# Performance work log

Measured on AMD Instinct MI355X. Metric: run time of the kernel, lower is better.

Reference implementation:

```python
import jax, jax.numpy as jnp
import numpy as np
from jax import lax

DIM = 128
HEADS = 2
SR = 4
HID = 512  # 4 * DIM
DROPKEY_P = 0.1


def _ln(x, g, b, eps=1e-5):
    m = jnp.mean(x, axis=-1, keepdims=True)
    v = jnp.var(x, axis=-1, keepdims=True)
    return (x - m) / jnp.sqrt(v + eps) * g + b


def _block(x, H, W, params, key):
    (n1g, n1b, qw, kvw, srw, srb, sng, snb, pw, pb,
     n2g, n2b, f1w, f1b, dww, dwb, f2w, f2b) = params
    B, N, C = x.shape
    dh = C // HEADS
    scale = dh ** -0.5
    # --- spatial-reduction attention ---
    h = _ln(x, n1g, n1b)
    q = (h @ qw.T).reshape(B, N, HEADS, dh).transpose(0, 2, 1, 3)  # [B,h,N,dh]
    xi = h.transpose(0, 2, 1).reshape(B, C, H, W)
    xs = lax.conv_general_dilated(xi, srw, (SR, SR), 'VALID',
                                  dimension_numbers=('NCHW', 'OIHW', 'NCHW'))
    xs = xs + srb[None, :, None, None]
    Np = (H // SR) * (W // SR)
    xs = xs.reshape(B, C, Np).transpose(0, 2, 1)  # [B,N',C]
    xs = _ln(xs, sng, snb)
    kv = (xs @ kvw.T).reshape(B, Np, 2, HEADS, dh).transpose(2, 0, 3, 1, 4)
    k, v = kv[0], kv[1]  # [B,h,N',dh]
    attn = jnp.einsum('bhnd,bhmd->bhnm', q, k) * scale
    # dropkey: bernoulli(p) mask pushed to -1e12 before softmax (always applied)
    mask = jax.random.bernoulli(key, DROPKEY_P, attn.shape)
    attn = attn + mask.astype(attn.dtype) * (-1e12)
    attn = jax.nn.softmax(attn, axis=-1)
    o = jnp.einsum('bhnm,bhmd->bhnd', attn, v).transpose(0, 2, 1, 3).reshape(B, N, C)
    x = x + o @ pw.T + pb
    # --- MLP with depthwise conv ---
    h2 = _ln(x, n2g, n2b)
    h2 = h2 @ f1w.T + f1b  # [B,N,HID]
    hi = h2.transpose(0, 2, 1).reshape(B, HID, H, W)
    hi = lax.conv_general_dilated(hi, dww, (1, 1), 'SAME',
                                  feature_group_count=HID,
                                  dimension_numbers=('NCHW', 'OIHW', 'NCHW'))
    hi = hi + dwb[None, :, None, None]
    h2 = hi.reshape(B, HID, N).transpose(0, 2, 1)
    h2 = jax.nn.gelu(h2, approximate=False)
    x = x + h2 @ f2w.T + f2b
    return x


def setup_inputs() -> dict:
    key = jax.random.key(0)
    ks = jax.random.split(key, 10)
    p = {}
    p['x'] = jax.random.normal(ks[0], (16, 2 * DIM, 56, 56), jnp.float32)
    p['concat_w'] = jax.random.normal(ks[1], (DIM, 2 * DIM), jnp.float32) * 0.02
    p['concat_b'] = jnp.zeros((DIM,), jnp.float32)
    # two Blocks -> leading dim 2 on all per-block params
    p['norm1_g'] = jnp.ones((2, DIM), jnp.float32)
    p['norm1_b'] = jnp.zeros((2, DIM), jnp.float32)
    p['q_w'] = jax.random.normal(ks[2], (2, DIM, DIM), jnp.float32) * 0.02
    p['kv_w'] = jax.random.normal(ks[3], (2, 2 * DIM, DIM), jnp.float32) * 0.02
    p['sr_w'] = jax.random.normal(ks[4], (2, DIM, DIM, SR, SR), jnp.float32) * 0.03
    p['sr_b'] = jnp.zeros((2, DIM), jnp.float32)
    p['srn_g'] = jnp.ones((2, DIM), jnp.float32)
    p['srn_b'] = jnp.zeros((2, DIM), jnp.float32)
    p['proj_w'] = jax.random.normal(ks[5], (2, DIM, DIM), jnp.float32) * 0.02
    p['proj_b'] = jnp.zeros((2, DIM), jnp.float32)
    p['norm2_g'] = jnp.ones((2, DIM), jnp.float32)
    p['norm2_b'] = jnp.zeros((2, DIM), jnp.float32)
    p['fc1_w'] = jax.random.normal(ks[6], (2, HID, DIM), jnp.float32) * 0.02
    p['fc1_b'] = jnp.zeros((2, HID), jnp.float32)
    p['dw_w'] = jax.random.normal(ks[7], (2, HID, 1, 3, 3), jnp.float32) * 0.1
    p['dw_b'] = jnp.zeros((2, HID), jnp.float32)
    p['fc2_w'] = jax.random.normal(ks[8], (2, DIM, HID), jnp.float32) * 0.02
    p['fc2_b'] = jnp.zeros((2, DIM), jnp.float32)
    return p


def reference(x, concat_w, concat_b, norm1_g, norm1_b, q_w, kv_w, sr_w, sr_b,
              srn_g, srn_b, proj_w, proj_b, norm2_g, norm2_b, fc1_w, fc1_b,
              dw_w, dw_b, fc2_w, fc2_b):
    b, c, h, w = x.shape
    xs = x.transpose(0, 2, 3, 1).reshape(b, h * w, c)
    xs = xs @ concat_w.T + concat_b  # [B,N,DIM]
    mkey = jax.random.key(42)
    stacked = (norm1_g, norm1_b, q_w, kv_w, sr_w, sr_b, srn_g, srn_b, proj_w,
               proj_b, norm2_g, norm2_b, fc1_w, fc1_b, dw_w, dw_b, fc2_w, fc2_b)
    for i in range(2):
        params_i = tuple(p[i] for p in stacked)
        xs = _block(xs, h, w, params_i, jax.random.fold_in(mkey, i))
    return xs.reshape(b, h, w, DIM).transpose(0, 3, 1, 2)
```

## Files before the change

kernel.cpp:

```cpp
#include <hip/hip_runtime.h>
#include <stdint.h>

typedef __attribute__((ext_vector_type(8))) short short8;
typedef __attribute__((ext_vector_type(4))) float f32x4;
typedef __attribute__((ext_vector_type(2))) float f32x2;
typedef unsigned short u16;
typedef uint32_t u32;
typedef unsigned long long u64;

__host__ __device__ static inline void threefry(u32 k0, u32 k1, u32 x0, u32 x1,
                                                u32* o0, u32* o1) {
  u32 ks2 = k0 ^ k1 ^ 0x1BD11BDAu;
  x0 += k0; x1 += k1;
#define TF_RR(r) { x0 += x1; x1 = (x1 << (r)) | (x1 >> (32 - (r))); x1 ^= x0; }
  TF_RR(13) TF_RR(15) TF_RR(26) TF_RR(6)
  x0 += k1;  x1 += ks2 + 1u;
  TF_RR(17) TF_RR(29) TF_RR(16) TF_RR(24)
  x0 += ks2; x1 += k0 + 2u;
  TF_RR(13) TF_RR(15) TF_RR(26) TF_RR(6)
  x0 += k0;  x1 += k1 + 3u;
  TF_RR(17) TF_RR(29) TF_RR(16) TF_RR(24)
  x0 += k1;  x1 += ks2 + 4u;
  TF_RR(13) TF_RR(15) TF_RR(26) TF_RR(6)
  x0 += ks2; x1 += k0 + 5u;
#undef TF_RR
  *o0 = x0; *o1 = x1;
}

__device__ static inline float bf2f(u16 u) {
  union { u32 i; float f; } v; v.i = ((u32)u) << 16; return v.f;
}
__device__ static inline u16 f2bf(float f) {
  union { float f; u32 i; } v; v.f = f;
  u32 x = v.i;
  return (u16)((x + 0x7FFFu + ((x >> 16) & 1u)) >> 16);
}
__device__ static inline float lo_bf(u32 w) {
  union { u32 i; float f; } v; v.i = w << 16; return v.f;
}
__device__ static inline float hi_bf(u32 w) {
  union { u32 i; float f; } v; v.i = w & 0xFFFF0000u; return v.f;
}
__device__ static inline bool is_f32(const u32* ng) { return ng[0] == 0x3F800000u; }

typedef const uint32_t __attribute__((address_space(1)))* gas_ptr;
typedef uint32_t __attribute__((address_space(3)))* las_ptr;
__device__ static inline void gld16(const u16* g, u16* l) {
  __builtin_amdgcn_global_load_lds((gas_ptr)(const void*)g, (las_ptr)(void*)l, 16, 0, 0);
}

#define MASK_HALF 9834496u

__global__ __launch_bounds__(256) void mask_gen2(u32* __restrict__ MSK2, u32 k0, u32 k1) {
  int t = blockIdx.x * 256 + threadIdx.x;
  if (t >= 351232) return;
  int w = t % 7;
  int rowbh = t / 7;
  u32 base = (u32)rowbh * 196u + (u32)w * 32u;
  int kmax = 196 - w * 32;
  if (kmax > 32) kmax = 32;
  u32 bits0 = 0, bits1 = 0;
  for (int j = 0; j < kmax; j++) {
    u32 o0, o1;
    threefry(k0, k1, base + (u32)j, base + (u32)j + MASK_HALF, &o0, &o1);
    union { u32 u; float f; } u0, u1;
    u0.u = (o0 >> 9) | 0x3F800000u;
    u1.u = (o1 >> 9) | 0x3F800000u;
    if (u0.f - 1.0f < 0.1f) bits0 |= (1u << j);
    if (u1.f - 1.0f < 0.1f) bits1 |= (1u << j);
  }
  MSK2[(size_t)rowbh * 7 + w] = bits0;
  MSK2[(size_t)(rowbh + 50176) * 7 + w] = bits1;
}

struct PtrTab { const void* p[20]; };
#define ARENA_N 963968
#define VT_WORDS 229376

__global__ __launch_bounds__(256) void convert_params(PtrTab tab, u16* __restrict__ arena,
                                                      u32* __restrict__ VT) {
  const int cum[21] = {0, 32768, 32896, 33152, 33408, 66176, 131712, 656000, 656256,
                       656512, 656768, 689536, 689792, 690048, 690304, 821376, 822400,
                       831616, 832640, 963712, 963968};
  int idx = blockIdx.x * 256 + threadIdx.x;
  if (idx >= ARENA_N) {
    int v = idx - ARENA_N;
    if (v < VT_WORDS) VT[v] = 0;
    return;
  }
  bool f32m = (((const u32*)tab.p[2])[0] == 0x3F800000u);
  int t = 0;
  while (idx >= cum[t + 1]) t++;
  int local = idx - cum[t];
  if (t == 16) {
    int blk = local / 4608, r = local - blk * 4608;
    int wi = r >> 9, c = r & 511;
    local = blk * 4608 + c * 9 + wi;
  }
  u16 v;
  if (f32m) v = f2bf(((const float*)tab.p[t])[local]);
  else      v = ((const u16*)tab.p[t])[local];
  arena[idx] = v;
}

__global__ __launch_bounds__(256) void transpose_in(const void* __restrict__ Xin,
                                                    const u32* __restrict__ ng,
                                                    u16* __restrict__ Xt) {
  bool f32m = is_f32(ng);
  __shared__ u16 tile[64][65];
  int n0 = blockIdx.x * 64, c0 = blockIdx.y * 64, b = blockIdx.z;
  int tx = threadIdx.x & 63, ty = threadIdx.x >> 6;
  if (f32m) {
    const float* src = (const float*)Xin + (size_t)b * 256 * 3136;
#pragma unroll
    for (int i = 0; i < 16; i++) {
      int cl = i * 4 + ty;
      tile[cl][tx] = f2bf(src[(size_t)(c0 + cl) * 3136 + n0 + tx]);
    }
  } else {
    const u16* src = (const u16*)Xin + (size_t)b * 256 * 3136;
#pragma unroll
    for (int i = 0; i < 16; i++) {
      int cl = i * 4 + ty;
      tile[cl][tx] = src[(size_t)(c0 + cl) * 3136 + n0 + tx];
    }
  }
  __syncthreads();
  u16* dst = Xt + (size_t)b * 3136 * 256;
#pragma unroll
  for (int i = 0; i < 16; i++) {
    int nl = i * 4 + ty;
    dst[(size_t)(n0 + nl) * 256 + c0 + tx] = tile[tx][nl];
  }
}

__global__ __launch_bounds__(256) void transpose_out(const float* __restrict__ X,
                                                     const u32* __restrict__ ng,
                                                     void* __restrict__ Out) {
  bool f32m = is_f32(ng);
  __shared__ float tile[64][65];
  int n0 = blockIdx.x * 64, d0 = blockIdx.y * 64, b = blockIdx.z;
  int tx = threadIdx.x & 63, ty = threadIdx.x >> 6;
#pragma unroll
  for (int i = 0; i < 16; i++) {
    int nl = i * 4 + ty;
    tile[nl][tx] = X[((size_t)b * 3136 + n0 + nl) * 128 + d0 + tx];
  }
  __syncthreads();
#pragma unroll
  for (int i = 0; i < 16; i++) {
    int dl = i * 4 + ty;
    size_t o = ((size_t)b * 128 + d0 + dl) * 3136 + n0 + tx;
    if (f32m) ((float*)Out)[o] = tile[tx][dl];
    else      ((u16*)Out)[o]   = f2bf(tile[tx][dl]);
  }
}

__global__ __launch_bounds__(256) void im2col_sr(const u16* __restrict__ H,
                                                 u16* __restrict__ Acol) {
  int t = blockIdx.x * 256 + threadIdx.x;
  int c = t & 127;
  int rest = t >> 7;
  int ij = rest & 15;
  int row = rest >> 4;
  int i = ij >> 2, j = ij & 3;
  int bb = row / 196, pp = row - bb * 196;
  int ph = pp / 14, pw = pp - ph * 14;
  int n = (4 * ph + i) * 56 + 4 * pw + j;
  Acol[(size_t)row * 2048 + c * 16 + ij] = H[((size_t)bb * 3136 + n) * 128 + c];
}

__global__ __launch_bounds__(256) __attribute__((amdgpu_waves_per_eu(2, 4)))
void gemm_tiled(const u16* __restrict__ A,
                const u16* __restrict__ W,
                const u16* __restrict__ bias,
                float* __restrict__ outF,
                u16* __restrict__ outB,
                u16* __restrict__ outVT,
                int M, int N, int K, int mode) {
  __shared__ __align__(16) u16 smem[16896];
  u16* AlsP = smem;
  u16* BlsP = smem + 8192;
  int n0 = blockIdx.y * 128, m0 = blockIdx.x * 128;
  int tid = threadIdx.x, wv = tid >> 6, lane = tid & 63;
  int wr = wv >> 1, wc = wv & 1;
  int l15 = lane & 15, hh = lane >> 4, lk = hh * 8;
  int srow = wv * 32 + (lane >> 2);
  int scol = (lane & 3) * 8;

  f32x4 acc[4][4];
#pragma unroll
  for (int m = 0; m < 4; m++)
#pragma unroll
    for (int n = 0; n < 4; n++) acc[m][n] = (f32x4){0.f, 0.f, 0.f, 0.f};

#define STAGE(buf, k0)                                                          \
  {                                                                             \
    _Pragma("unroll") for (int i = 0; i < 2; i++) {                             \
      int ar = m0 + srow + i * 16;                                              \
      if (ar >= M) ar = M - 1;                                                  \
      gld16(A + (size_t)ar * K + (k0) + scol,                                   \
            AlsP + (buf) * 4096 + (wv * 32 + i * 16) * 32);                     \
      int br = n0 + srow + i * 16;                                              \
      gld16(W + (size_t)br * K + (k0) + scol,                                   \
            BlsP + (buf) * 4096 + (wv * 32 + i * 16) * 32);                     \
    }                                                                           \
  }

  int nt = K >> 5;
  STAGE(0, 0);
  int cur = 0;
  for (int t = 0; t < nt; t++) {
    __syncthreads();
    if (t + 1 < nt) STAGE(cur ^ 1, (t + 1) * 32);
    short8 af[4], bf[4];
#pragma unroll
    for (int m = 0; m < 4; m++)
      af[m] = *(const short8*)(AlsP + cur * 4096 + (wr * 64 + m * 16 + l15) * 32 + lk);
#pragma unroll
    for (int n = 0; n < 4; n++)
      bf[n] = *(const short8*)(BlsP + cur * 4096 + (wc * 64 + n * 16 + l15) * 32 + lk);
#pragma unroll
    for (int m = 0; m < 4; m++)
#pragma unroll
      for (int n = 0; n < 4; n++)
        acc[m][n] = __builtin_amdgcn_mfma_f32_16x16x32_bf16(af[m], bf[n], acc[m][n], 0, 0, 0);
    cur ^= 1;
  }
#undef STAGE

  if (mode == 0) {
    __syncthreads();
#pragma unroll
    for (int n = 0; n < 4; n++) {
      int col = wc * 64 + n * 16 + l15;
      float bv = bias ? bf2f(bias[n0 + col]) : 0.0f;
#pragma unroll
      for (int m = 0; m < 4; m++) {
        int rbase = wr * 64 + m * 16 + hh * 4;
#pragma unroll
        for (int r = 0; r < 4; r++)
          smem[(rbase + r) * 132 + col] = f2bf(acc[m][n][r] + bv);
      }
    }
    __syncthreads();
#pragma unroll
    for (int p = 0; p < 8; p++) {
      int row = p * 16 + (tid >> 4);
      int colb = (tid & 15) * 8;
      int grow = m0 + row;
      if (grow < M) {
        short8 v = *(const short8*)&smem[row * 132 + colb];
        *(short8*)(outB + (size_t)grow * N + n0 + colb) = v;
      }
    }
    return;
  }

#pragma unroll
  for (int n = 0; n < 4; n++) {
    int col = n0 + wc * 64 + n * 16 + l15;
    float bv = bias ? bf2f(bias[col]) : 0.0f;
#pragma unroll
    for (int m = 0; m < 4; m++) {
      int rbase = m0 + wr * 64 + m * 16 + hh * 4;
#pragma unroll
      for (int r = 0; r < 4; r++) {
        int row = rbase + r;
        if (row < M) {
          float v = acc[m][n][r] + bv;
          if (mode == 1) outF[(size_t)row * N + col] = v;
          else if (mode == 2) outF[(size_t)row * N + col] += v;
          else {
            if (col < 128) outB[(size_t)row * 128 + col] = f2bf(v);
            else {
              int hd = (col - 128) >> 6, d = (col - 128) & 63;
              int b = row / 196, key = row - b * 196;
              outVT[(size_t)((b * 2 + hd) * 64 + d) * 224 + key] = f2bf(v);
            }
          }
        }
      }
    }
  }
}

__global__ __launch_bounds__(256) __attribute__((amdgpu_waves_per_eu(2, 4)))
void gemm_n128(const u16* __restrict__ A,
               const u16* __restrict__ W,
               const u16* __restrict__ bias,
               float* __restrict__ outF,
               u16* __restrict__ outB,
               const u16* __restrict__ lnG,
               const u16* __restrict__ lnB,
               u16* __restrict__ outH,
               int M, int K, int mode) {
  __shared__ __align__(16) u16 smem[12288];
  __shared__ float sumsA[64][4];
  __shared__ float sumsB[64][4];
  u16* Als = smem;
  u16* Bls = smem + 4096;
  int m0 = blockIdx.y * 64;
  int tid = threadIdx.x, wv = tid >> 6, lane = tid & 63;
  int l15 = lane & 15, hq = lane >> 4, lk = hq * 8;
  int scol = (lane & 3) * 8;

  f32x4 acc[4][2];
#pragma unroll
  for (int m = 0; m < 4; m++)
#pragma unroll
    for (int n = 0; n < 2; n++) acc[m][n] = (f32x4){0.f, 0.f, 0.f, 0.f};

#define STAGE(buf, k0)                                                          \
  {                                                                             \
    int ar = m0 + wv * 16 + (lane >> 2);                                        \
    if (ar >= M) ar = M - 1;                                                    \
    gld16(A + (size_t)ar * K + (k0) + scol, Als + (buf) * 2048 + wv * 512);     \
    _Pragma("unroll") for (int i = 0; i < 2; i++) {                             \
      int br = wv * 32 + i * 16 + (lane >> 2);                                  \
      gld16(W + (size_t)br * K + (k0) + scol,                                   \
            Bls + (buf) * 4096 + wv * 1024 + i * 512);                          \
    }                                                                           \
  }

  int nt = K >> 5;
  STAGE(0, 0);
  int cur = 0;
  for (int t = 0; t < nt; t++) {
    __syncthreads();
    if (t + 1 < nt) STAGE(cur ^ 1, (t + 1) * 32);
    short8 af[4], bf[2];
#pragma unroll
    for (int m = 0; m < 4; m++)
      af[m] = *(const short8*)(Als + cur * 2048 + (m * 16 + l15) * 32 + lk);
#pragma unroll
    for (int n = 0; n < 2; n++)
      bf[n] = *(const short8*)(Bls + cur * 4096 + (wv * 32 + n * 16 + l15) * 32 + lk);
#pragma unroll
    for (int m = 0; m < 4; m++)
#pragma unroll
      for (int n = 0; n < 2; n++)
        acc[m][n] = __builtin_amdgcn_mfma_f32_16x16x32_bf16(af[m], bf[n], acc[m][n], 0, 0, 0);
    cur ^= 1;
  }
#undef STAGE

  if (mode == 2) {
#pragma unroll
    for (int n = 0; n < 2; n++) {
      int col = wv * 32 + n * 16 + l15;
      float bv = bias ? bf2f(bias[col]) : 0.0f;
#pragma unroll
      for (int m = 0; m < 4; m++) {
        int rbase = m0 + m * 16 + hq * 4;
#pragma unroll
        for (int r = 0; r < 4; r++)
          outF[(size_t)(rbase + r) * 128 + col] += acc[m][n][r] + bv;
      }
    }
    return;
  }

  if (mode >= 4) {
#pragma unroll
    for (int n = 0; n < 2; n++) {
      int col = wv * 32 + n * 16 + l15;
      float bv = bias ? bf2f(bias[col]) : 0.0f;
#pragma unroll
      for (int m = 0; m < 4; m++) {
        int rbase = m0 + m * 16 + hq * 4;
#pragma unroll
        for (int r = 0; r < 4; r++) {
          float v = acc[m][n][r] + bv;
          if (mode == 5) v += outF[(size_t)(rbase + r) * 128 + col];
          acc[m][n][r] = v;
          outF[(size_t)(rbase + r) * 128 + col] = v;
        }
      }
    }
#pragma unroll
    for (int m = 0; m < 4; m++) {
#pragma unroll
      for (int r = 0; r < 4; r++) {
        float a = acc[m][0][r] + acc[m][1][r];
        float b = acc[m][0][r] * acc[m][0][r] + acc[m][1][r] * acc[m][1][r];
#pragma unroll
        for (int d = 1; d < 16; d <<= 1) {
          a += __shfl_xor(a, d);
          b += __shfl_xor(b, d);
        }
        if (l15 == 0) {
          int lrow = m * 16 + hq * 4 + r;
          sumsA[lrow][wv] = a;
          sumsB[lrow][wv] = b;
        }
      }
    }
    __syncthreads();
#pragma unroll
    for (int m = 0; m < 4; m++) {
#pragma unroll
      for (int r = 0; r < 4; r++) {
        int lrow = m * 16 + hq * 4 + r;
        float t1 = sumsA[lrow][0] + sumsA[lrow][1] + sumsA[lrow][2] + sumsA[lrow][3];
        float t2 = sumsB[lrow][0] + sumsB[lrow][1] + sumsB[lrow][2] + sumsB[lrow][3];
        float mean = t1 * 0.0078125f;
        float var = t2 * 0.0078125f - mean * mean;
        float inv = 1.0f / sqrtf(var + 1e-5f);
#pragma unroll
        for (int n = 0; n < 2; n++) {
          int col = wv * 32 + n * 16 + l15;
          float g = bf2f(lnG[col]), bb2 = bf2f(lnB[col]);
          smem[lrow * 132 + col] = f2bf((acc[m][n][r] - mean) * inv * g + bb2);
        }
      }
    }
    __syncthreads();
#pragma unroll
    for (int p = 0; p < 4; p++) {
      int row = p * 16 + (tid >> 4);
      int colb = (tid & 15) * 8;
      short8 v = *(const short8*)&smem[row * 132 + colb];
      *(short8*)(outH + (size_t)(m0 + row) * 128 + colb) = v;
    }
    return;
  }

  __syncthreads();
#pragma unroll
  for (int n = 0; n < 2; n++) {
    int col = wv * 32 + n * 16 + l15;
    float bv = bias ? bf2f(bias[col]) : 0.0f;
#pragma unroll
    for (int m = 0; m < 4; m++) {
      int rbase = m * 16 + hq * 4;
#pragma unroll
      for (int r = 0; r < 4; r++)
        smem[(rbase + r) * 132 + col] = f2bf(acc[m][n][r] + bv);
    }
  }
  __syncthreads();
#pragma unroll
  for (int p = 0; p < 4; p++) {
    int row = p * 16 + (tid >> 4);
    int colb = (tid & 15) * 8;
    short8 v = *(const short8*)&smem[row * 132 + colb];
    *(short8*)(outB + (size_t)(m0 + row) * 128 + colb) = v;
  }
}

__global__ __launch_bounds__(256) void gemm_splitk(const u16* __restrict__ A,
                                                   const u16* __restrict__ W,
                                                   float* __restrict__ PS,
                                                   int M, int N, int K) {
  __shared__ __align__(16) u16 Als[2][4096];
  __shared__ __align__(16) u16 Bls[2][4096];
  int n0 = blockIdx.x * 128, m0 = blockIdx.y * 128, ks = blockIdx.z;
  int tid = threadIdx.x, wv = tid >> 6, lane = tid & 63;
  int wr = wv >> 1, wc = wv & 1;
  int l15 = lane & 15, lk = (lane >> 4) * 8;
  int srow = wv * 32 + (lane >> 2);
  int scol = (lane & 3) * 8;

  f32x4 acc[4][4];
#pragma unroll
  for (int m = 0; m < 4; m++)
#pragma unroll
    for (int n = 0; n < 4; n++) acc[m][n] = (f32x4){0.f, 0.f, 0.f, 0.f};

#define STAGE(buf, k0)                                                          \
  {                                                                             \
    _Pragma("unroll") for (int i = 0; i < 2; i++) {                             \
      int ar = m0 + srow + i * 16;                                              \
      if (ar >= M) ar = M - 1;                                                  \
      gld16(A + (size_t)ar * K + (k0) + scol,                                   \
            &Als[buf][(wv * 32 + i * 16) * 32]);                                \
      int br = n0 + srow + i * 16;                                              \
      gld16(W + (size_t)br * K + (k0) + scol,                                   \
            &Bls[buf][(wv * 32 + i * 16) * 32]);                                \
    }                                                                           \
  }

  int kbeg = ks * 128;
  STAGE(0, kbeg);
  int cur = 0;
  for (int t = 0; t < 4; t++) {
    __syncthreads();
    if (t + 1 < 4) STAGE(cur ^ 1, kbeg + (t + 1) * 32);
    short8 af[4], bf[4];
#pragma unroll
    for (int m = 0; m < 4; m++)
      af[m] = *(const short8*)(&Als[cur][(wr * 64 + m * 16 + l15) * 32 + lk]);
#pragma unroll
    for (int n = 0; n < 4; n++)
      bf[n] = *(const short8*)(&Bls[cur][(wc * 64 + n * 16 + l15) * 32 + lk]);
#pragma unroll
    for (int m = 0; m < 4; m++)
#pragma unroll
      for (int n = 0; n < 4; n++)
        acc[m][n] = __builtin_amdgcn_mfma_f32_16x16x32_bf16(af[m], bf[n], acc[m][n], 0, 0, 0);
    cur ^= 1;
  }
#undef STAGE

  float* myPS = PS + (size_t)ks * M * N;
#pragma unroll
  for (int n = 0; n < 4; n++) {
    int col = n0 + wc * 64 + n * 16 + l15;
#pragma unroll
    for (int m = 0; m < 4; m++) {
      int rbase = m0 + wr * 64 + m * 16 + (lane >> 4) * 4;
#pragma unroll
      for (int r = 0; r < 4; r++) {
        int row = rbase + r;
        if (row < M) myPS[(size_t)row * N + col] = acc[m][n][r];
      }
    }
  }
}

__global__ __launch_bounds__(256) void splitk_reduce_ln(const float* __restrict__ PS,
                                                        const u16* __restrict__ bias,
                                                        const u16* __restrict__ G,
                                                        const u16* __restrict__ Bi,
                                                        u16* __restrict__ XSN) {
  __shared__ float red[4][2];
  int tid = threadIdx.x;
  int row = blockIdx.x * 2 + (tid >> 7);
  int col = tid & 127;
  int t = row * 128 + col;
  float s = bf2f(bias[col]);
#pragma unroll
  for (int k = 0; k < 16; k++) s += PS[(size_t)k * 401408 + t];
  float s1 = s, s2 = s * s;
#pragma unroll
  for (int d = 1; d < 64; d <<= 1) {
    s1 += __shfl_xor(s1, d);
    s2 += __shfl_xor(s2, d);
  }
  int wv = tid >> 6;
  if ((tid & 63) == 0) { red[wv][0] = s1; red[wv][1] = s2; }
  __syncthreads();
  int other = wv ^ 1;
  float t1 = red[wv][0] + red[other][0];
  float t2 = red[wv][1] + red[other][1];
  float mean = t1 * 0.0078125f;
  float var = t2 * 0.0078125f - mean * mean;
  float inv = 1.0f / sqrtf(var + 1e-5f);
  XSN[t] = f2bf((s - mean) * inv * bf2f(G[col]) + bf2f(Bi[col]));
}

__global__ __launch_bounds__(256) __attribute__((amdgpu_waves_per_eu(2, 4)))
void attn_kernel(const u16* __restrict__ Q,
                 const u16* __restrict__ Kb,
                 const u16* __restrict__ VT,
                 const u32* __restrict__ M2,
                 u16* __restrict__ O) {
  __shared__ __align__(16) u16 smA[14848];
  int t = blockIdx.x;
  int tp = (t & 7) * 196 + (t >> 3);
  int bh = tp / 49, qt = tp - bh * 49;
  int b = bh >> 1, hd = bh & 1;
  int q0 = qt * 64;
  int tid = threadIdx.x;

  int wv = tid >> 6, lane = tid & 63;
  int l15 = lane & 15, h = lane >> 4, lk = h * 8;

  {
    const u16* ksrc = Kb + (size_t)b * 196 * 128 + hd * 64;
    for (int idx = tid; idx < 1568; idx += 256) {
      int row = idx >> 3, ch = idx & 7;
      short8 v = *(const short8*)(ksrc + (size_t)row * 128 + ch * 8);
      *(short8*)&smA[row * 68 + ch * 8] = v;
    }
  }

  const u16* qp = Q + ((size_t)(b * 3136 + q0 + wv * 16 + l15) * 128) + hd * 64 + lk;
  short8 aq0 = *(const short8*)(qp);
  short8 aq1 = *(const short8*)(qp + 32);
  int rowg = q0 + wv * 16 + h * 4;

  u32 mwv[4][7];
  const u32* mwbase = M2 + (size_t)(bh * 3136 + rowg) * 7;
#pragma unroll
  for (int r = 0; r < 4; r++)
#pragma unroll
    for (int w = 0; w < 7; w++) mwv[r][w] = mwbase[r * 7 + w];

  __syncthreads();

  float sarr[13][4];
#pragma unroll
  for (int cc = 0; cc < 13; cc++) {
    int key = cc * 16 + l15;
    int keyc = key > 195 ? 195 : key;
    short8 kb0 = *(const short8*)&smA[keyc * 68 + lk];
    short8 kb1 = *(const short8*)&smA[keyc * 68 + 32 + lk];
    f32x4 s = {0.f, 0.f, 0.f, 0.f};
    s = __builtin_amdgcn_mfma_f32_16x16x32_bf16(aq0, kb0, s, 0, 0, 0);
    s = __builtin_amdgcn_mfma_f32_16x16x32_bf16(aq1, kb1, s, 0, 0, 0);
#pragma unroll
    for (int r = 0; r < 4; r++) sarr[cc][r] = s[r] * 0.125f;
  }

#pragma unroll
  for (int cc = 0; cc < 13; cc++) {
    bool keyok = (cc * 16 + l15) < 196;
    int pos = (cc & 3) * 16 + l15;
#pragma unroll
    for (int r = 0; r < 4; r++) {
      u64 mm = (cc < 4) ? ((u64)mwv[r][0] | ((u64)mwv[r][1] << 32))
             : (cc < 8) ? ((u64)mwv[r][2] | ((u64)mwv[r][3] << 32))
             : (cc < 12) ? ((u64)mwv[r][4] | ((u64)mwv[r][5] << 32))
                         : ((u64)mwv[r][6]);
      bool drop = (mm >> pos) & 1ull;
      if (!keyok || drop) sarr[cc][r] = -3.0e38f;
    }
  }

  float mx[4] = {sarr[0][0], sarr[0][1], sarr[0][2], sarr[0][3]};
#pragma unroll
  for (int cc = 1; cc < 13; cc++)
#pragma unroll
    for (int r = 0; r < 4; r++) mx[r] = fmaxf(mx[r], sarr[cc][r]);
#pragma unroll
  for (int d = 1; d < 16; d <<= 1)
#pragma unroll
    for (int r = 0; r < 4; r++) mx[r] = fmaxf(mx[r], __shfl_xor(mx[r], d));
  float sm[4] = {0.f, 0.f, 0.f, 0.f};
#pragma unroll
  for (int cc = 0; cc < 13; cc++)
#pragma unroll
    for (int r = 0; r < 4; r++) {
      float p = __expf(sarr[cc][r] - mx[r]);
      sarr[cc][r] = p;
      sm[r] += p;
    }
#pragma unroll
  for (int d = 1; d < 16; d <<= 1)
#pragma unroll
    for (int r = 0; r < 4; r++) sm[r] += __shfl_xor(sm[r], d);
  float inv[4];
#pragma unroll
  for (int r = 0; r < 4; r++)
    asm("v_rcp_f32 %0, %1" : "=v"(inv[r]) : "v"(sm[r]));

  __syncthreads();

#pragma unroll
  for (int cc = 0; cc < 13; cc++)
#pragma unroll
    for (int r = 0; r < 4; r++)
      smA[(wv * 16 + h * 4 + r) * 232 + cc * 16 + l15] = f2bf(sarr[cc][r] * inv[r]);
#pragma unroll
  for (int rj = 0; rj < 4; rj++) smA[(wv * 16 + l15) * 232 + 208 + h * 4 + rj] = 0;

  const u16* vbase = VT + (size_t)(bh * 64) * 224;
  short8 vw[4];
#pragma unroll
  for (int i = 0; i < 4; i++) {
    vw[i] = *(const short8*)(vbase + (size_t)(0 * 16 + l15) * 224 + i * 32 + lk);
  }
#pragma unroll
  for (int dc = 0; dc < 4; dc++) {
    f32x4 oa = {0.f, 0.f, 0.f, 0.f};
#pragma unroll
    for (int kc = 0; kc < 7; kc++) {
      int i = dc * 7 + kc;
      short8 bv = vw[i & 3];
      if (i + 4 < 28) {
        int i2 = i + 4;
        int dc2 = i2 / 7, kc2 = i2 - dc2 * 7;
        vw[i & 3] =
            *(const short8*)(vbase + (size_t)(dc2 * 16 + l15) * 224 + kc2 * 32 + lk);
      }
      short8 a = *(const short8*)&smA[(wv * 16 + l15) * 232 + kc * 32 + lk];
      oa = __builtin_amdgcn_mfma_f32_16x16x32_bf16(a, bv, oa, 0, 0, 0);
    }
#pragma unroll
    for (int r = 0; r < 4; r++) {
      O[((size_t)(b * 3136 + rowg + r) * 128) + hd * 64 + dc * 16 + l15] = f2bf(oa[r]);
    }
  }
}

__global__ __launch_bounds__(256) __attribute__((amdgpu_waves_per_eu(2, 4)))
void dwconv_gelu(const u16* __restrict__ H2,
                 const u16* __restrict__ Wdw,
                 const u16* __restrict__ Bdw,
                 u16* __restrict__ Out) {
  int tid = threadIdx.x;
  int wv = tid >> 6, lane = tid & 63;
  int sb = blockIdx.x;
  int wg = (sb & 7) * 392 + (sb >> 3);
  int strip = wg * 4 + wv;
  int bb = strip / 784;
  int s = strip - bb * 784;
  int y = s / 14, x0 = (s - y * 14) * 4;
  int c0 = lane * 8;

  f32x2 wf[9][4];
#pragma unroll
  for (int t9 = 0; t9 < 9; t9++) {
    short8 w8 = *(const short8*)(Wdw + t9 * 512 + c0);
#pragma unroll
    for (int p = 0; p < 4; p++) {
      u32 w = ((const u32*)&w8)[p];
      wf[t9][p] = (f32x2){lo_bf(w), hi_bf(w)};
    }
  }
  f32x2 acc[4][4];
  {
    short8 b8 = *(const short8*)(Bdw + c0);
#pragma unroll
    for (int p = 0; p < 4; p++) {
      u32 w = ((const u32*)&b8)[p];
      f32x2 bv = {lo_bf(w), hi_bf(w)};
#pragma unroll
      for (int q = 0; q < 4; q++) acc[q][p] = bv;
    }
  }

  const u16* base = H2 + ((size_t)bb * 3136) * 512 + c0;
#pragma unroll
  for (int di = -1; di <= 1; di++) {
    int y2 = y + di;
    if (y2 < 0 || y2 >= 56) continue;
    const u16* rowp = base + (size_t)(y2 * 56) * 512;
#pragma unroll
    for (int j = 0; j < 6; j++) {
      int c = x0 - 1 + j;
      if (c < 0 || c > 55) continue;
      short8 h8 = *(const short8*)(rowp + (size_t)c * 512);
      f32x2 hf[4];
#pragma unroll
      for (int p = 0; p < 4; p++) {
        u32 w = ((const u32*)&h8)[p];
        hf[p] = (f32x2){lo_bf(w), hi_bf(w)};
      }
      int wrow = (di + 1) * 3;
#pragma unroll
      for (int q = 0; q < 4; q++) {
        int dx = j - 1 - q;
        if (dx < -1 || dx > 1) continue;
#pragma unroll
        for (int p = 0; p < 4; p++) acc[q][p] += hf[p] * wf[wrow + dx + 1][p];
      }
    }
  }

  size_t obase = ((size_t)(bb * 3136 + y * 56 + x0)) * 512 + c0;
#pragma unroll
  for (int q = 0; q < 4; q++) {
    short8 ov;
#pragma unroll
    for (int p = 0; p < 4; p++) {
      float g2[2];
#pragma unroll
      for (int e = 0; e < 2; e++) {
        float v = acc[q][p][e];
        float tt = v * v;
        float yn = v * (-2.3022088f - 0.1029434f * tt);
        float ex;
        asm("v_exp_f32 %0, %1" : "=v"(ex) : "v"(yn));
        float den = 1.0f + ex;
        float sg;
        asm("v_rcp_f32 %0, %1" : "=v"(sg) : "v"(den));
        g2[e] = v * sg;
      }
      u32 pk;
      asm("v_cvt_pk_bf16_f32 %0, %1, %2" : "=v"(pk) : "v"(g2[0]), "v"(g2[1]));
      ((u32*)&ov)[p] = pk;
    }
    *(short8*)(Out + obase + (size_t)q * 512) = ov;
  }
}

__global__ __launch_bounds__(256) void fill_sentinel(void* __restrict__ Out,
                                                     const u32* __restrict__ ng, int n) {
  bool f32m = is_f32(ng);
  int t = blockIdx.x * 256 + threadIdx.x;
  if (t >= n) return;
  if (f32m) ((float*)Out)[t] = 12345.0f;
  else      ((u16*)Out)[t]   = f2bf(12345.0f);
}

extern "C" void kernel_launch(void* const* d_in, const int* in_sizes, int n_in,
                              void* d_out, int out_size, void* d_ws, size_t ws_size,
                              hipStream_t stream) {
  (void)in_sizes; (void)n_in;
  const u32* ng = (const u32*)d_in[3];

  const size_t o_X   = 0;
  const size_t o_H   = 25690112;
  const size_t o_R   = o_H + 12845056;
  const size_t o_Q   = o_R;
  const size_t o_O   = o_R + 12845056;
  const size_t o_Xt  = o_R + 25690112;
  const size_t o_H2C = o_R;
  const size_t o_H2  = o_R + 51380224;
  const size_t o_XSN = o_H2 + 51380224;
  const size_t o_KB  = o_XSN + 802816;
  const size_t o_VT  = o_KB + 802816;
  const size_t o_M2  = o_VT + 917504;
  const size_t o_AR  = o_M2 + 2809856;
  const size_t NEED  = o_AR + (size_t)ARENA_N * 2;

  if (ws_size < NEED) {
    fill_sentinel<<<(out_size + 255) / 256, 256, 0, stream>>>(d_out, ng, out_size);
    return;
  }

  char* ws = (char*)d_ws;
  float* X  = (float*)(ws + o_X);
  u16* H    = (u16*)(ws + o_H);
  u16* Qb   = (u16*)(ws + o_Q);
  u16* Ob   = (u16*)(ws + o_O);
  u16* Xt   = (u16*)(ws + o_Xt);
  u16* H2C  = (u16*)(ws + o_H2C);
  u16* H2   = (u16*)(ws + o_H2);
  float* PS = (float*)(ws + o_H2);
  u16* XSN  = (u16*)(ws + o_XSN);
  u16* Kb   = (u16*)(ws + o_KB);
  u16* VT   = (u16*)(ws + o_VT);
  u32* MSK2 = (u32*)(ws + o_M2);
  u16* AR   = (u16*)(ws + o_AR);

  PtrTab tab;
  for (int j = 0; j < 20; j++) tab.p[j] = d_in[j + 1];
  convert_params<<<(ARENA_N + VT_WORDS + 255) / 256, 256, 0, stream>>>(tab, AR, (u32*)VT);

  u16* ACW  = AR + 0;      u16* ACB  = AR + 32768;
  u16* AN1G = AR + 32896;  u16* AN1B = AR + 33152;
  u16* AQW  = AR + 33408;  u16* AKVW = AR + 66176;
  u16* ASRW = AR + 131712; u16* ASRB = AR + 656000;
  u16* ASNG = AR + 656256; u16* ASNB = AR + 656512;
  u16* APW  = AR + 656768; u16* APB  = AR + 689536;
  u16* AN2G = AR + 689792; u16* AN2B = AR + 690048;
  u16* AF1W = AR + 690304; u16* AF1B = AR + 821376;
  u16* ADWW = AR + 822400; u16* ADWB = AR + 831616;
  u16* AF2W = AR + 832640; u16* AF2B = AR + 963712;

  transpose_in<<<dim3(49, 4, 16), 256, 0, stream>>>(d_in[0], ng, Xt);
  gemm_n128<<<dim3(1, 784), 256, 0, stream>>>(Xt, ACW, ACB, X, nullptr,
                                              AN1G, AN1B, H, 50176, 256, 4);

  for (int i = 0; i < 2; i++) {
    u32 fk0, fk1;
    threefry(0u, 42u, 0u, (u32)i, &fk0, &fk1);

    gemm_n128<<<dim3(1, 784), 256, 0, stream>>>(H, AQW + i * 16384, nullptr, nullptr,
                                                Qb, nullptr, nullptr, nullptr,
                                                50176, 128, 0);
    im2col_sr<<<25088, 256, 0, stream>>>(H, Xt);
    gemm_splitk<<<dim3(1, 25, 16), 256, 0, stream>>>(Xt, ASRW + i * 262144, PS,
                                                     3136, 128, 2048);
    mask_gen2<<<1372, 256, 0, stream>>>(MSK2, fk0, fk1);
    splitk_reduce_ln<<<1568, 256, 0, stream>>>(PS, ASRB + i * 128,
                                               ASNG + i * 128, ASNB + i * 128, XSN);

    gemm_tiled<<<dim3(25, 2), 256, 0, stream>>>(XSN, AKVW + i * 32768, nullptr, nullptr,
                                                Kb, VT, 3136, 256, 128, 3);
    attn_kernel<<<1568, 256, 0, stream>>>(Qb, Kb, VT, MSK2, Ob);
    gemm_n128<<<dim3(1, 784), 256, 0, stream>>>(Ob, APW + i * 16384, APB + i * 128,
                                                X, nullptr,
                                                AN2G + i * 128, AN2B + i * 128, H,
                                                50176, 128, 5);
    gemm_tiled<<<dim3(392, 4), 256, 0, stream>>>(H, AF1W + i * 65536, AF1B + i * 512,
                                                 nullptr, H2, nullptr,
                                                 50176, 512, 128, 0);
    dwconv_gelu<<<3136, 256, 0, stream>>>(H2, ADWW + i * 4608, ADWB + i * 512, H2C);
    if (i == 0) {
      gemm_n128<<<dim3(1, 784), 256, 0, stream>>>(H2C, AF2W, AF2B, X, nullptr,
                                                  AN1G + 128, AN1B + 128, H,
                                                  50176, 512, 5);
    } else {
      gemm_n128<<<dim3(1, 784), 256, 0, stream>>>(H2C, AF2W + 65536, AF2B + 128,
                                                  X, nullptr, nullptr, nullptr, nullptr,
                                                  50176, 512, 2);
    }
  }

  transpose_out<<<dim3(49, 2, 16), 256, 0, stream>>>(X, ng, d_out);
}
```

Before: 481.2 us.

## Fuse Q projection into LayerNorm-epilogue GEMM and pad LDS row stride

The Q projection GEMM now runs inside the epilogue of the GEMM that produces the LayerNorm output H. The normalized tile already sitting in LDS is reused as the A operand, and qW is read straight from global memory. This removes a separate 784-block launch and the re-read of H per block, at the cost of extra work, register pressure and global B-fragment loads in the fused kernel. The LDS row stride also changes from 132 to 136 elements across epilogues, which alters bank mapping for the 16-byte reads.

```diff
diff --git a/kernel.cpp b/kernel.cpp
--- a/kernel.cpp
+++ b/kernel.cpp
@@ -178,7 +178,7 @@
                 u16* __restrict__ outB,
                 u16* __restrict__ outVT,
                 int M, int N, int K, int mode) {
-  __shared__ __align__(16) u16 smem[16896];
+  __shared__ __align__(16) u16 smem[17408];
   u16* AlsP = smem;
   u16* BlsP = smem + 8192;
   int n0 = blockIdx.y * 128, m0 = blockIdx.x * 128;
@@ -240,7 +240,7 @@
         int rbase = wr * 64 + m * 16 + hh * 4;
 #pragma unroll
         for (int r = 0; r < 4; r++)
-          smem[(rbase + r) * 132 + col] = f2bf(acc[m][n][r] + bv);
+          smem[(rbase + r) * 136 + col] = f2bf(acc[m][n][r] + bv);
       }
     }
     __syncthreads();
@@ -250,7 +250,7 @@
       int colb = (tid & 15) * 8;
       int grow = m0 + row;
       if (grow < M) {
-        short8 v = *(const short8*)&smem[row * 132 + colb];
+        short8 v = *(const short8*)&smem[row * 136 + colb];
         *(short8*)(outB + (size_t)grow * N + n0 + colb) = v;
       }
     }
@@ -294,6 +294,8 @@
                const u16* __restrict__ lnG,
                const u16* __restrict__ lnB,
                u16* __restrict__ outH,
+               const u16* __restrict__ qW,
+               u16* __restrict__ outQ,
                int M, int K, int mode) {
   __shared__ __align__(16) u16 smem[12288];
   __shared__ float sumsA[64][4];
@@ -411,7 +413,7 @@
         for (int n = 0; n < 2; n++) {
           int col = wv * 32 + n * 16 + l15;
           float g = bf2f(lnG[col]), bb2 = bf2f(lnB[col]);
-          smem[lrow * 132 + col] = f2bf((acc[m][n][r] - mean) * inv * g + bb2);
+          smem[lrow * 136 + col] = f2bf((acc[m][n][r] - mean) * inv * g + bb2);
         }
       }
     }
@@ -420,8 +422,52 @@
     for (int p = 0; p < 4; p++) {
       int row = p * 16 + (tid >> 4);
       int colb = (tid & 15) * 8;
-      short8 v = *(const short8*)&smem[row * 132 + colb];
+      short8 v = *(const short8*)&smem[row * 136 + colb];
       *(short8*)(outH + (size_t)(m0 + row) * 128 + colb) = v;
+    }
+
+    if (qW) {
+#pragma unroll
+      for (int m = 0; m < 4; m++)
+#pragma unroll
+        for (int n = 0; n < 2; n++) acc[m][n] = (f32x4){0.f, 0.f, 0.f, 0.f};
+#pragma unroll
+      for (int kc = 0; kc < 4; kc++) {
+        short8 af[4], bf[2];
+#pragma unroll
+        for (int m = 0; m < 4; m++)
+          af[m] = *(const short8*)&smem[(m * 16 + l15) * 136 + kc * 32 + lk];
+#pragma unroll
+        for (int n = 0; n < 2; n++)
+          bf[n] = *(const short8*)(qW + (size_t)(wv * 32 + n * 16 + l15) * 128 +
+                                   kc * 32 + lk);
+#pragma unroll
+        for (int m = 0; m < 4; m++)
+#pragma unroll
+          for (int n = 0; n < 2; n++)
+            acc[m][n] =
+                __builtin_amdgcn_mfma_f32_16x16x32_bf16(af[m], bf[n], acc[m][n], 0, 0, 0);
+      }
+      __syncthreads();
+#pragma unroll
+      for (int n = 0; n < 2; n++) {
+        int col = wv * 32 + n * 16 + l15;
+#pragma unroll
+        for (int m = 0; m < 4; m++) {
+          int rbase = m * 16 + hq * 4;
+#pragma unroll
+          for (int r = 0; r < 4; r++)
+            smem[(rbase + r) * 136 + col] = f2bf(acc[m][n][r]);
+        }
+      }
+      __syncthreads();
+#pragma unroll
+      for (int p = 0; p < 4; p++) {
+        int row = p * 16 + (tid >> 4);
+        int colb = (tid & 15) * 8;
+        short8 v = *(const short8*)&smem[row * 136 + colb];
+        *(short8*)(outQ + (size_t)(m0 + row) * 128 + colb) = v;
+      }
     }
     return;
   }
@@ -436,7 +482,7 @@
       int rbase = m * 16 + hq * 4;
 #pragma unroll
       for (int r = 0; r < 4; r++)
-        smem[(rbase + r) * 132 + col] = f2bf(acc[m][n][r] + bv);
+        smem[(rbase + r) * 136 + col] = f2bf(acc[m][n][r] + bv);
     }
   }
   __syncthreads();
@@ -444,7 +490,7 @@
   for (int p = 0; p < 4; p++) {
     int row = p * 16 + (tid >> 4);
     int colb = (tid & 15) * 8;
-    short8 v = *(const short8*)&smem[row * 132 + colb];
+    short8 v = *(const short8*)&smem[row * 136 + colb];
     *(short8*)(outB + (size_t)(m0 + row) * 128 + colb) = v;
   }
 }
@@ -844,15 +890,13 @@
 
   transpose_in<<<dim3(49, 4, 16), 256, 0, stream>>>(d_in[0], ng, Xt);
   gemm_n128<<<dim3(1, 784), 256, 0, stream>>>(Xt, ACW, ACB, X, nullptr,
-                                              AN1G, AN1B, H, 50176, 256, 4);
+                                              AN1G, AN1B, H, AQW, Qb,
+                                              50176, 256, 4);
 
   for (int i = 0; i < 2; i++) {
     u32 fk0, fk1;
     threefry(0u, 42u, 0u, (u32)i, &fk0, &fk1);
 
-    gemm_n128<<<dim3(1, 784), 256, 0, stream>>>(H, AQW + i * 16384, nullptr, nullptr,
-                                                Qb, nullptr, nullptr, nullptr,
-                                                50176, 128, 0);
     im2col_sr<<<25088, 256, 0, stream>>>(H, Xt);
     gemm_splitk<<<dim3(1, 25, 16), 256, 0, stream>>>(Xt, ASRW + i * 262144, PS,
                                                      3136, 128, 2048);
@@ -866,7 +910,7 @@
     gemm_n128<<<dim3(1, 784), 256, 0, stream>>>(Ob, APW + i * 16384, APB + i * 128,
                                                 X, nullptr,
                                                 AN2G + i * 128, AN2B + i * 128, H,
-                                                50176, 128, 5);
+                                                nullptr, nullptr, 50176, 128, 5);
     gemm_tiled<<<dim3(392, 4), 256, 0, stream>>>(H, AF1W + i * 65536, AF1B + i * 512,
                                                  nullptr, H2, nullptr,
                                                  50176, 512, 128, 0);
@@ -874,11 +918,11 @@
     if (i == 0) {
       gemm_n128<<<dim3(1, 784), 256, 0, stream>>>(H2C, AF2W, AF2B, X, nullptr,
                                                   AN1G + 128, AN1B + 128, H,
-                                                  50176, 512, 5);
+                                                  AQW + 16384, Qb, 50176, 512, 5);
     } else {
       gemm_n128<<<dim3(1, 784), 256, 0, stream>>>(H2C, AF2W + 65536, AF2B + 128,
                                                   X, nullptr, nullptr, nullptr, nullptr,
-                                                  50176, 512, 2);
+                                                  nullptr, nullptr, 50176, 512, 2);
     }
   }
 
```

After: 471.2 us. 2.1% less time.
